# Kernel tuning notes

Measured on AMD Instinct MI355X. Metric: run time of the kernel, lower is better.

Reference implementation:

```python
import jax, jax.numpy as jnp
import numpy as np

N_NODES = 100000
N_EDGES = 2000000
D = 128
HIDDEN = 128


def setup_inputs() -> dict:
    key = jax.random.key(0)
    k_src, k_dst, k_idx, k_w1, k_w2 = jax.random.split(key, 5)
    src = jax.random.normal(k_src, (N_NODES, D), dtype=jnp.float32)
    dst = jax.random.normal(k_dst, (N_NODES, D), dtype=jnp.float32)
    edge_label_index = jax.random.randint(k_idx, (2, N_EDGES), 0, N_NODES, dtype=jnp.int64)
    # Kaiming-ish init for the two linear layers
    W1 = jax.random.normal(k_w1, (D, HIDDEN), dtype=jnp.float32) / np.sqrt(D)
    b1 = jnp.zeros((HIDDEN,), dtype=jnp.float32)
    W2 = jax.random.normal(k_w2, (HIDDEN, 1), dtype=jnp.float32) / np.sqrt(HIDDEN)
    b2 = jnp.zeros((1,), dtype=jnp.float32)
    return {"src": src, "dst": dst, "edge_label_index": edge_label_index,
            "W1": W1, "b1": b1, "W2": W2, "b2": b2}


def reference(src, dst, edge_label_index, W1, b1, W2, b2):
    row = edge_label_index[0]
    col = edge_label_index[1]
    # gather endpoint embeddings and fuse with elementwise product: [E, D]
    z = src[row] * dst[col]
    # 2-layer MLP; dropout p=0 is the identity
    h = jax.nn.relu(z @ W1 + b1)           # [E, HIDDEN]
    out = h @ W2 + b2                       # [E, 1]
    return out.reshape(-1)                  # [E]
```

## Files before the change

kernel.cpp:

```cpp
#include <hip/hip_runtime.h>
#include <hip/hip_bf16.h>

typedef __attribute__((ext_vector_type(8))) short short8;
typedef __attribute__((ext_vector_type(16))) float f32x16;

#define BLOCK 256
#define GTILE 32

__device__ __forceinline__ int swz16(int row, int boff) {
    return (row << 8) + (boff ^ ((row & 15) << 4));
}
__device__ __forceinline__ int swzH(int row, int boff) {
    return (row << 7) + (boff ^ ((row & 7) << 4));
}

__global__ __launch_bounds__(256) void cvt_bf16_kernel(
    const float* __restrict__ a, const float* __restrict__ b,
    __hip_bfloat16* __restrict__ oa, __hip_bfloat16* __restrict__ ob, int n)
{
    const int i = blockIdx.x * blockDim.x + threadIdx.x;
    const int stride = gridDim.x * blockDim.x;
    const float4* a4 = (const float4*)a;
    const float4* b4 = (const float4*)b;
    const int n8 = n >> 3;
    for (int j = i; j < n8; j += stride) {
        float4 x0 = a4[2 * j], x1 = a4[2 * j + 1];
        float4 y0 = b4[2 * j], y1 = b4[2 * j + 1];
        union { __hip_bfloat16 h[8]; uint4 u; } pa, pb;
        pa.h[0]=__float2bfloat16(x0.x); pa.h[1]=__float2bfloat16(x0.y);
        pa.h[2]=__float2bfloat16(x0.z); pa.h[3]=__float2bfloat16(x0.w);
        pa.h[4]=__float2bfloat16(x1.x); pa.h[5]=__float2bfloat16(x1.y);
        pa.h[6]=__float2bfloat16(x1.z); pa.h[7]=__float2bfloat16(x1.w);
        pb.h[0]=__float2bfloat16(y0.x); pb.h[1]=__float2bfloat16(y0.y);
        pb.h[2]=__float2bfloat16(y0.z); pb.h[3]=__float2bfloat16(y0.w);
        pb.h[4]=__float2bfloat16(y1.x); pb.h[5]=__float2bfloat16(y1.y);
        pb.h[6]=__float2bfloat16(y1.z); pb.h[7]=__float2bfloat16(y1.w);
        ((uint4*)oa)[j] = pa.u;
        ((uint4*)ob)[j] = pb.u;
    }
    for (int j = (n8 << 3) + i; j < n; j += stride) {
        oa[j] = __float2bfloat16(a[j]);
        ob[j] = __float2bfloat16(b[j]);
    }
}

template<bool BF16G>
__global__ __launch_bounds__(BLOCK, 3) void edge_mlp_kernel(
    const float* __restrict__ srcf, const float* __restrict__ dstf,
    const __hip_bfloat16* __restrict__ srcb, const __hip_bfloat16* __restrict__ dstb,
    const int*   __restrict__ eli,
    const float* __restrict__ W1, const float* __restrict__ b1,
    const float* __restrict__ W2, const float* __restrict__ b2,
    float* __restrict__ out, int E)
{
    __shared__ __align__(16) char lds[49152];

    const int tid  = threadIdx.x;
    const int lane = tid & 63;
    const int w    = tid >> 6;
    const int n32  = lane & 31;
    const int half = lane >> 5;
    const int rq8  = lane >> 3;
    const int cl   = lane & 7;

    for (int idx = tid; idx < 128 * 128; idx += BLOCK) {
        int k = idx >> 7, n = idx & 127;
        *(__hip_bfloat16*)(lds + swz16(n, k * 2)) = __float2bfloat16(W1[idx]);
    }
    int probe = eli[2 * (lane & 31) + 1];
    unsigned long long bl = __ballot(lane < 32 && probe != 0);
    const int i64f = (bl == 0ull) ? 1 : 0;
    __syncthreads();

    char* zb = lds + 32768 + (w << 12);

    float b1s[4], w2s[4];
    #pragma unroll
    for (int cb = 0; cb < 4; ++cb) {
        b1s[cb] = b1[cb * 32 + n32];
        w2s[cb] = W2[cb * 32 + n32];
    }
    const float bias2 = b2[0];

    const int ngroups = (E + GTILE - 1) / GTILE;
    const int step = gridDim.x * 4;
    int g = blockIdx.x * 4 + w;
    if (g >= ngroups) return;

    auto idxload = [&](int gg) -> int {
        gg = gg < ngroups ? gg : ngroups - 1;
        int e = gg * GTILE + n32; if (e >= E) e = E - 1;
        size_t off = half ? (size_t)E + (size_t)e : (size_t)e;
        return i64f ? eli[2 * off] : eli[off];
    };

    short8 sv[4], dv[4];
    auto loadP = [&](int iv, int p) {
        const short8* s8 = (const short8*)srcb;
        const short8* d8 = (const short8*)dstb;
        #pragma unroll
        for (int i = 0; i < 4; ++i) {
            int R = i * 8 + rq8;
            int r = __shfl(iv, R, 64);
            int c = __shfl(iv, 32 + R, 64);
            sv[i] = s8[(size_t)r * 16 + p * 8 + cl];
            dv[i] = d8[(size_t)c * 16 + p * 8 + cl];
        }
    };
    auto writeP = [&]() {
        #pragma unroll
        for (int i = 0; i < 4; ++i) {
            int R = i * 8 + rq8;
            union { __hip_bfloat16 h[8]; short8 v; } pr;
            #pragma unroll
            for (int j = 0; j < 8; ++j) {
                float fs = __bfloat162float(((const __hip_bfloat16*)&sv[i])[j]);
                float fd = __bfloat162float(((const __hip_bfloat16*)&dv[i])[j]);
                pr.h[j] = __float2bfloat16(fs * fd);
            }
            *(short8*)(zb + swzH(R, cl * 16)) = pr.v;
        }
    };
    auto stagePhaseF = [&](int iv, int p) {
        const float4* s4 = (const float4*)srcf;
        const float4* d4 = (const float4*)dstf;
        #pragma unroll
        for (int i = 0; i < 4; ++i) {
            int R = i * 8 + rq8;
            int r = __shfl(iv, R, 64);
            int c = __shfl(iv, 32 + R, 64);
            float4 a0 = s4[(size_t)r * 32 + p * 16 + cl * 2];
            float4 a1 = s4[(size_t)r * 32 + p * 16 + cl * 2 + 1];
            float4 c0 = d4[(size_t)c * 32 + p * 16 + cl * 2];
            float4 c1 = d4[(size_t)c * 32 + p * 16 + cl * 2 + 1];
            union { __hip_bfloat16 h[8]; short8 v; } pr;
            pr.h[0] = __float2bfloat16(a0.x * c0.x);
            pr.h[1] = __float2bfloat16(a0.y * c0.y);
            pr.h[2] = __float2bfloat16(a0.z * c0.z);
            pr.h[3] = __float2bfloat16(a0.w * c0.w);
            pr.h[4] = __float2bfloat16(a1.x * c1.x);
            pr.h[5] = __float2bfloat16(a1.y * c1.y);
            pr.h[6] = __float2bfloat16(a1.z * c1.z);
            pr.h[7] = __float2bfloat16(a1.w * c1.w);
            *(short8*)(zb + swzH(R, cl * 16)) = pr.v;
        }
    };

    int iv_cur = idxload(g);
    if constexpr (BF16G) loadP(iv_cur, 0);
    int iv_nxt = idxload(g + step);

    for (; g < ngroups; g += step) {
        asm volatile("" ::: "memory");

        f32x16 acc[4];
        #pragma unroll
        for (int cb = 0; cb < 4; ++cb)
            #pragma unroll
            for (int j = 0; j < 16; ++j)
                acc[cb][j] = 0.f;

        if constexpr (BF16G) { writeP(); loadP(iv_cur, 1); }
        else                 stagePhaseF(iv_cur, 0);
        asm volatile("" ::: "memory");
        __builtin_amdgcn_s_setprio(1);
        #pragma unroll
        for (int kk = 0; kk < 4; ++kk) {
            short8 af = *(const short8*)(zb + swzH(n32, kk * 32 + half * 16));
            #pragma unroll
            for (int cb = 0; cb < 4; ++cb) {
                short8 bf = *(const short8*)(lds + swz16(cb * 32 + n32,
                                                         kk * 32 + half * 16));
                acc[cb] = __builtin_amdgcn_mfma_f32_32x32x16_bf16(af, bf, acc[cb], 0, 0, 0);
            }
        }
        __builtin_amdgcn_s_setprio(0);
        asm volatile("" ::: "memory");

        if constexpr (BF16G) {
            writeP();
            loadP(iv_nxt, 0);
            iv_cur = iv_nxt;
            iv_nxt = idxload(g + 2 * step);
        } else {
            stagePhaseF(iv_cur, 1);
            iv_cur = iv_nxt;
            iv_nxt = idxload(g + 2 * step);
        }
        asm volatile("" ::: "memory");
        __builtin_amdgcn_s_setprio(1);
        #pragma unroll
        for (int kk = 0; kk < 4; ++kk) {
            short8 af = *(const short8*)(zb + swzH(n32, kk * 32 + half * 16));
            #pragma unroll
            for (int cb = 0; cb < 4; ++cb) {
                short8 bf = *(const short8*)(lds + swz16(cb * 32 + n32,
                                                         (kk + 4) * 32 + half * 16));
                acc[cb] = __builtin_amdgcn_mfma_f32_32x32x16_bf16(af, bf, acc[cb], 0, 0, 0);
            }
        }
        __builtin_amdgcn_s_setprio(0);
        asm volatile("" ::: "memory");

        #pragma unroll
        for (int r = 0; r < 16; ++r) {
            float p = 0.f;
            #pragma unroll
            for (int cb = 0; cb < 4; ++cb) {
                float h = acc[cb][r] + b1s[cb];
                h = fmaxf(h, 0.f);
                p = fmaf(h, w2s[cb], p);
            }
            int R = (r & 3) + 8 * (r >> 2) + 4 * half;
            *(float*)(zb + ((R << 7) + ((n32 << 2) ^ ((R & 7) << 4)))) = p;
        }
        asm volatile("" ::: "memory");
        float tot = 0.f;
        #pragma unroll
        for (int j = 0; j < 4; ++j) {
            float4 v = *(const float4*)(zb + ((n32 << 7) +
                         ((half * 64 + j * 16) ^ ((n32 & 7) << 4))));
            tot += v.x + v.y + v.z + v.w;
        }
        tot += __shfl_xor(tot, 32, 64);
        int e = g * GTILE + n32;
        if (half == 0 && e < E)
            __builtin_nontemporal_store(tot + bias2, &out[e]);
    }
}

extern "C" void kernel_launch(void* const* d_in, const int* in_sizes, int n_in,
                              void* d_out, int out_size, void* d_ws, size_t ws_size,
                              hipStream_t stream) {
    const float* src = (const float*)d_in[0];
    const float* dst = (const float*)d_in[1];
    const int*   eli = (const int*)d_in[2];
    const float* W1  = (const float*)d_in[3];
    const float* b1  = (const float*)d_in[4];
    const float* W2  = (const float*)d_in[5];
    const float* b2  = (const float*)d_in[6];
    float* out = (float*)d_out;

    const int E = in_sizes[2] / 2;
    const int nsrc = in_sizes[0];
    const size_t need = (size_t)(in_sizes[0] + in_sizes[1]) * sizeof(__hip_bfloat16);
    const int ngroups = (E + GTILE - 1) / GTILE;
    int nblocks = (ngroups + 3) / 4;
    int grid = nblocks < 768 ? nblocks : 768;

    if (ws_size >= need) {
        __hip_bfloat16* srcb = (__hip_bfloat16*)d_ws;
        __hip_bfloat16* dstb = srcb + nsrc;
        cvt_bf16_kernel<<<dim3(2048), dim3(256), 0, stream>>>(src, dst, srcb, dstb, nsrc);
        edge_mlp_kernel<true><<<dim3(grid), dim3(BLOCK), 0, stream>>>(
            src, dst, srcb, dstb, eli, W1, b1, W2, b2, out, E);
    } else {
        edge_mlp_kernel<false><<<dim3(grid), dim3(BLOCK), 0, stream>>>(
            src, dst, (const __hip_bfloat16*)nullptr, (const __hip_bfloat16*)nullptr,
            eli, W1, b1, W2, b2, out, E);
    }
}
```

Before: 186.7 us.

## Switch to 16-edge tiles with 16x16x32 MFMA and two-deep gather prefetch

Edge tiles shrink from 32 to 16 edges per wave, and the 32x32x16 MFMA becomes 16x16x32. All 128 features of a tile are staged at once instead of in two halves. The bf16 gather path now double-buffers two full tiles in registers, so loads for tile g+2 overlap compute on tile g. The final W2 reduction uses wave shuffles instead of an LDS round trip. The cost is more loop iterations, more register pressure from two buffered tiles, and less MFMA work per instruction.

```diff
diff --git a/kernel.cpp b/kernel.cpp
--- a/kernel.cpp
+++ b/kernel.cpp
@@ -2,10 +2,10 @@
 #include <hip/hip_bf16.h>
 
 typedef __attribute__((ext_vector_type(8))) short short8;
-typedef __attribute__((ext_vector_type(16))) float f32x16;
+typedef __attribute__((ext_vector_type(4))) float f32x4;
 
 #define BLOCK 256
-#define GTILE 32
+#define GTILE 16
 
 __device__ __forceinline__ int swz16(int row, int boff) {
     return (row << 8) + (boff ^ ((row & 15) << 4));
@@ -58,8 +58,8 @@
     const int tid  = threadIdx.x;
     const int lane = tid & 63;
     const int w    = tid >> 6;
-    const int n32  = lane & 31;
-    const int half = lane >> 5;
+    const int rr   = lane & 15;
+    const int kgrp = lane >> 4;
     const int rq8  = lane >> 3;
     const int cl   = lane & 7;
 
@@ -74,11 +74,11 @@
 
     char* zb = lds + 32768 + (w << 12);
 
-    float b1s[4], w2s[4];
+    float b1s[8], w2s[8];
     #pragma unroll
-    for (int cb = 0; cb < 4; ++cb) {
-        b1s[cb] = b1[cb * 32 + n32];
-        w2s[cb] = W2[cb * 32 + n32];
+    for (int cb = 0; cb < 8; ++cb) {
+        b1s[cb] = b1[cb * 16 + rr];
+        w2s[cb] = W2[cb * 16 + rr];
     }
     const float bias2 = b2[0];
 
@@ -89,143 +89,133 @@
 
     auto idxload = [&](int gg) -> int {
         gg = gg < ngroups ? gg : ngroups - 1;
-        int e = gg * GTILE + n32; if (e >= E) e = E - 1;
-        size_t off = half ? (size_t)E + (size_t)e : (size_t)e;
+        int e = gg * GTILE + rr; if (e >= E) e = E - 1;
+        size_t off = (lane < 32) ? (size_t)e : (size_t)E + (size_t)e;
         return i64f ? eli[2 * off] : eli[off];
     };
 
-    short8 sv[4], dv[4];
-    auto loadP = [&](int iv, int p) {
+    auto loadT = [&](int iv, short8 (&s)[4], short8 (&d)[4]) {
         const short8* s8 = (const short8*)srcb;
         const short8* d8 = (const short8*)dstb;
         #pragma unroll
         for (int i = 0; i < 4; ++i) {
-            int R = i * 8 + rq8;
-            int r = __shfl(iv, R, 64);
-            int c = __shfl(iv, 32 + R, 64);
-            sv[i] = s8[(size_t)r * 16 + p * 8 + cl];
-            dv[i] = d8[(size_t)c * 16 + p * 8 + cl];
-        }
-    };
-    auto writeP = [&]() {
+            int hr = i * 8 + rq8;
+            int e  = hr >> 1, h = hr & 1;
+            int r = __shfl(iv, e, 64);
+            int c = __shfl(iv, 32 + e, 64);
+            s[i] = s8[(size_t)r * 16 + h * 8 + cl];
+            d[i] = d8[(size_t)c * 16 + h * 8 + cl];
+        }
+    };
+    auto writeT = [&](const short8 (&s)[4], const short8 (&d)[4]) {
         #pragma unroll
         for (int i = 0; i < 4; ++i) {
-            int R = i * 8 + rq8;
+            int hr = i * 8 + rq8;
             union { __hip_bfloat16 h[8]; short8 v; } pr;
             #pragma unroll
             for (int j = 0; j < 8; ++j) {
-                float fs = __bfloat162float(((const __hip_bfloat16*)&sv[i])[j]);
-                float fd = __bfloat162float(((const __hip_bfloat16*)&dv[i])[j]);
+                float fs = __bfloat162float(((const __hip_bfloat16*)&s[i])[j]);
+                float fd = __bfloat162float(((const __hip_bfloat16*)&d[i])[j]);
                 pr.h[j] = __float2bfloat16(fs * fd);
             }
-            *(short8*)(zb + swzH(R, cl * 16)) = pr.v;
-        }
-    };
-    auto stagePhaseF = [&](int iv, int p) {
+            *(short8*)(zb + swzH(hr, cl * 16)) = pr.v;
+        }
+    };
+    auto stageF = [&](int iv) {
         const float4* s4 = (const float4*)srcf;
         const float4* d4 = (const float4*)dstf;
         #pragma unroll
         for (int i = 0; i < 4; ++i) {
-            int R = i * 8 + rq8;
-            int r = __shfl(iv, R, 64);
-            int c = __shfl(iv, 32 + R, 64);
-            float4 a0 = s4[(size_t)r * 32 + p * 16 + cl * 2];
-            float4 a1 = s4[(size_t)r * 32 + p * 16 + cl * 2 + 1];
-            float4 c0 = d4[(size_t)c * 32 + p * 16 + cl * 2];
-            float4 c1 = d4[(size_t)c * 32 + p * 16 + cl * 2 + 1];
-            union { __hip_bfloat16 h[8]; short8 v; } pr;
-            pr.h[0] = __float2bfloat16(a0.x * c0.x);
-            pr.h[1] = __float2bfloat16(a0.y * c0.y);
-            pr.h[2] = __float2bfloat16(a0.z * c0.z);
-            pr.h[3] = __float2bfloat16(a0.w * c0.w);
-            pr.h[4] = __float2bfloat16(a1.x * c1.x);
-            pr.h[5] = __float2bfloat16(a1.y * c1.y);
-            pr.h[6] = __float2bfloat16(a1.z * c1.z);
-            pr.h[7] = __float2bfloat16(a1.w * c1.w);
-            *(short8*)(zb + swzH(R, cl * 16)) = pr.v;
-        }
-    };
-
-    int iv_cur = idxload(g);
-    if constexpr (BF16G) loadP(iv_cur, 0);
-    int iv_nxt = idxload(g + step);
-
-    for (; g < ngroups; g += step) {
-        asm volatile("" ::: "memory");
-
-        f32x16 acc[4];
-        #pragma unroll
-        for (int cb = 0; cb < 4; ++cb)
+            int hr = i * 8 + rq8;
+            int e  = hr >> 1, h = hr & 1;
+            int r = __shfl(iv, e, 64);
+            int c = __shfl(iv, 32 + e, 64);
+            float4 a0 = s4[(size_t)r * 32 + h * 16 + cl * 2];
+            float4 a1 = s4[(size_t)r * 32 + h * 16 + cl * 2 + 1];
+            float4 c0 = d4[(size_t)c * 32 + h * 16 + cl * 2];
+            float4 c1 = d4[(size_t)c * 32 + h * 16 + cl * 2 + 1];
+            union { __hip_bfloat16 hh[8]; short8 v; } pr;
+            pr.hh[0] = __float2bfloat16(a0.x * c0.x);
+            pr.hh[1] = __float2bfloat16(a0.y * c0.y);
+            pr.hh[2] = __float2bfloat16(a0.z * c0.z);
+            pr.hh[3] = __float2bfloat16(a0.w * c0.w);
+            pr.hh[4] = __float2bfloat16(a1.x * c1.x);
+            pr.hh[5] = __float2bfloat16(a1.y * c1.y);
+            pr.hh[6] = __float2bfloat16(a1.z * c1.z);
+            pr.hh[7] = __float2bfloat16(a1.w * c1.w);
+            *(short8*)(zb + swzH(hr, cl * 16)) = pr.v;
+        }
+    };
+
+    auto compute = [&](int gg) {
+        f32x4 acc[8];
+        #pragma unroll
+        for (int cb = 0; cb < 8; ++cb) acc[cb] = (f32x4){0.f, 0.f, 0.f, 0.f};
+        __builtin_amdgcn_s_setprio(1);
+        #pragma unroll
+        for (int kk = 0; kk < 4; ++kk) {
+            short8 af = *(const short8*)(zb + swzH(rr * 2 + (kk >> 1),
+                                                   (kk & 1) * 64 + kgrp * 16));
             #pragma unroll
-            for (int j = 0; j < 16; ++j)
-                acc[cb][j] = 0.f;
-
-        if constexpr (BF16G) { writeP(); loadP(iv_cur, 1); }
-        else                 stagePhaseF(iv_cur, 0);
-        asm volatile("" ::: "memory");
-        __builtin_amdgcn_s_setprio(1);
-        #pragma unroll
-        for (int kk = 0; kk < 4; ++kk) {
-            short8 af = *(const short8*)(zb + swzH(n32, kk * 32 + half * 16));
-            #pragma unroll
-            for (int cb = 0; cb < 4; ++cb) {
-                short8 bf = *(const short8*)(lds + swz16(cb * 32 + n32,
-                                                         kk * 32 + half * 16));
-                acc[cb] = __builtin_amdgcn_mfma_f32_32x32x16_bf16(af, bf, acc[cb], 0, 0, 0);
+            for (int cb = 0; cb < 8; ++cb) {
+                short8 bf = *(const short8*)(lds + swz16(cb * 16 + rr,
+                                                         kk * 64 + kgrp * 16));
+                acc[cb] = __builtin_amdgcn_mfma_f32_16x16x32_bf16(af, bf, acc[cb], 0, 0, 0);
             }
         }
         __builtin_amdgcn_s_setprio(0);
-        asm volatile("" ::: "memory");
-
-        if constexpr (BF16G) {
-            writeP();
-            loadP(iv_nxt, 0);
-            iv_cur = iv_nxt;
-            iv_nxt = idxload(g + 2 * step);
-        } else {
-            stagePhaseF(iv_cur, 1);
-            iv_cur = iv_nxt;
-            iv_nxt = idxload(g + 2 * step);
-        }
-        asm volatile("" ::: "memory");
-        __builtin_amdgcn_s_setprio(1);
-        #pragma unroll
-        for (int kk = 0; kk < 4; ++kk) {
-            short8 af = *(const short8*)(zb + swzH(n32, kk * 32 + half * 16));
-            #pragma unroll
-            for (int cb = 0; cb < 4; ++cb) {
-                short8 bf = *(const short8*)(lds + swz16(cb * 32 + n32,
-                                                         (kk + 4) * 32 + half * 16));
-                acc[cb] = __builtin_amdgcn_mfma_f32_32x32x16_bf16(af, bf, acc[cb], 0, 0, 0);
-            }
-        }
-        __builtin_amdgcn_s_setprio(0);
-        asm volatile("" ::: "memory");
-
-        #pragma unroll
-        for (int r = 0; r < 16; ++r) {
+        #pragma unroll
+        for (int r = 0; r < 4; ++r) {
             float p = 0.f;
             #pragma unroll
-            for (int cb = 0; cb < 4; ++cb) {
+            for (int cb = 0; cb < 8; ++cb) {
                 float h = acc[cb][r] + b1s[cb];
                 h = fmaxf(h, 0.f);
                 p = fmaf(h, w2s[cb], p);
             }
-            int R = (r & 3) + 8 * (r >> 2) + 4 * half;
-            *(float*)(zb + ((R << 7) + ((n32 << 2) ^ ((R & 7) << 4)))) = p;
-        }
-        asm volatile("" ::: "memory");
-        float tot = 0.f;
-        #pragma unroll
-        for (int j = 0; j < 4; ++j) {
-            float4 v = *(const float4*)(zb + ((n32 << 7) +
-                         ((half * 64 + j * 16) ^ ((n32 & 7) << 4))));
-            tot += v.x + v.y + v.z + v.w;
-        }
-        tot += __shfl_xor(tot, 32, 64);
-        int e = g * GTILE + n32;
-        if (half == 0 && e < E)
-            __builtin_nontemporal_store(tot + bias2, &out[e]);
+            p += __shfl_xor(p, 1, 64);
+            p += __shfl_xor(p, 2, 64);
+            p += __shfl_xor(p, 4, 64);
+            p += __shfl_xor(p, 8, 64);
+            int e = gg * GTILE + kgrp * 4 + r;
+            if (rr == 0 && e < E)
+                __builtin_nontemporal_store(p + bias2, &out[e]);
+        }
+    };
+
+    if constexpr (BF16G) {
+        short8 svA[4], dvA[4], svB[4], dvB[4];
+        int iv0 = idxload(g);
+        int iv1 = idxload(g + step);
+        loadT(iv0, svA, dvA);
+        loadT(iv1, svB, dvB);
+        int iv2 = idxload(g + 2 * step);
+
+        while (true) {
+            asm volatile("" ::: "memory");
+            writeT(svA, dvA);
+            loadT(iv2, svA, dvA);
+            iv2 = idxload(g + 3 * step);
+            asm volatile("" ::: "memory");
+            compute(g);
+            g += step; if (g >= ngroups) break;
+
+            asm volatile("" ::: "memory");
+            writeT(svB, dvB);
+            loadT(iv2, svB, dvB);
+            iv2 = idxload(g + 3 * step);
+            asm volatile("" ::: "memory");
+            compute(g);
+            g += step; if (g >= ngroups) break;
+        }
+    } else {
+        for (; g < ngroups; g += step) {
+            asm volatile("" ::: "memory");
+            int iv = idxload(g);
+            stageF(iv);
+            asm volatile("" ::: "memory");
+            compute(g);
+        }
     }
 }
 
```

Result: faster. 178.0 us (-4.7%).
